# Performance work log

Hardware: AMD Instinct MI355X
Metric: run time of the kernel (lower is better)

Reference implementation:

```python
import math
import jax, jax.numpy as jnp
import numpy as np

CAPACITY_FACTOR = 1.0
MIN_CAPACITY = 8


def setup_inputs() -> dict:
    key = jax.random.key(0)
    k1, k2 = jax.random.split(key)
    s, d, e = 8192, 1024, 64
    inputs = jax.random.normal(k1, (s, d), dtype=jnp.float32)
    wg_weight = jax.random.normal(k2, (e, d), dtype=jnp.float32) * (1.0 / math.sqrt(d))
    return {"inputs": inputs, "wg_weight": wg_weight}


def reference(inputs, wg_weight):
    # gate projection (always fp32 in the original)
    logits = inputs.astype(jnp.float32) @ wg_weight.T  # [s, e]
    s, e = logits.shape
    # static capacity: ceil(s/e * capacity_factor), floored at min_capacity
    capacity = max(int(math.ceil(s / e * CAPACITY_FACTOR)), MIN_CAPACITY)

    gates = jax.nn.softmax(logits, axis=1)            # [s, e]
    indices = jnp.argmax(gates, axis=1)               # [s]
    mask = jax.nn.one_hot(indices, e, dtype=jnp.int32)  # [s, e]
    exp_counts = jnp.sum(mask, axis=0)                # [e]

    # load-balancing aux loss (uses mask BEFORE capacity dropping)
    me = jnp.mean(gates, axis=0)
    ce = jnp.mean(mask.astype(jnp.float32), axis=0)
    l_aux = jnp.sum(me * ce) * e

    # capacity dropping: with use_rts=False, topk over the binary mask keeps
    # the first `capacity` tokens routed to each expert, i.e. cumulative
    # position-in-expert < capacity
    positions = jnp.cumsum(mask, axis=0) - 1          # [s, e]
    mask = mask * (positions < capacity).astype(jnp.int32)

    locations = jnp.cumsum(mask, axis=0) - 1          # [s, e]
    locations_s = jnp.sum(locations * mask, axis=1)   # [s] slot per token

    gates = gates * mask.astype(jnp.float32)          # zero out dropped tokens
    locations_sc = jax.nn.one_hot(locations_s, capacity, dtype=jnp.float32)  # [s, c]
    combine_weights = jnp.einsum('se,sc->sec', gates, locations_sc)  # [s, e, c]
    dispatch_mask = combine_weights.astype(bool)
    return l_aux, combine_weights, dispatch_mask, exp_counts
```

## Files before the change

kernel.cpp:

```cpp
#include <hip/hip_runtime.h>
#include <cstdint>
#include <cstddef>

#define S 8192
#define Dm 1024
#define E 64
#define CAP 128
#define SEC 67108864ull

#define GEMM_BLOCKS 256
#define FILL_BLOCKS 1792
#define B0 16777217u
#define TCH 16777231u
#define CH 9363u
#define N4END 33554448u
#define WSCALE 4096.0f
#define INV_WSCALE (1.0f / 4096.0f)

typedef float f32x4 __attribute__((ext_vector_type(4)));
typedef _Float16 f16x4 __attribute__((ext_vector_type(4)));
typedef _Float16 f16x8 __attribute__((ext_vector_type(8)));

#define CV4(H, L, ROW, COL, V, SCALE) do {                                     \
    f16x4 hh, ll; float t_;                                                    \
    t_ = (V).x * (SCALE); hh[0] = (_Float16)t_; ll[0] = (_Float16)(t_ - (float)hh[0]); \
    t_ = (V).y * (SCALE); hh[1] = (_Float16)t_; ll[1] = (_Float16)(t_ - (float)hh[1]); \
    t_ = (V).z * (SCALE); hh[2] = (_Float16)t_; ll[2] = (_Float16)(t_ - (float)hh[2]); \
    t_ = (V).w * (SCALE); hh[3] = (_Float16)t_; ll[3] = (_Float16)(t_ - (float)hh[3]); \
    *(f16x4*)&H[ROW][COL] = hh;                                                \
    *(f16x4*)&L[ROW][COL] = ll;                                                \
} while (0)

__global__ __launch_bounds__(512) void k_main(const float* __restrict__ x,
                                              const float* __restrict__ w,
                                              float* __restrict__ gate,
                                              int* __restrict__ idx,
                                              float* __restrict__ me_part,
                                              int* __restrict__ cnt_g,
                                              float* __restrict__ la_ws,
                                              float* __restrict__ out) {
    int bid = blockIdx.x;
    int tid = threadIdx.x;
    if (bid < GEMM_BLOCKS) {
        __shared__ _Float16 Ah[32][72];
        __shared__ _Float16 Alo[32][72];
        __shared__ _Float16 Wh[64][72];
        __shared__ _Float16 Wlo[64][72];
        __shared__ float Sl[32][66];
        __shared__ float sm[32];
        __shared__ float sinv[32];
        __shared__ int sidx[32];
        int t0 = bid * 32;
        int ar = tid >> 4;
        int ac = (tid & 15) * 4;
        int wr = tid >> 3;
        int wc = (tid & 7) * 8;
        const float* asrc = x + (size_t)(t0 + ar) * Dm + ac;
        const float* wsrc = w + (size_t)wr * Dm + wc;

        int wv = tid >> 6;
        int l = tid & 63;
        int lr = l & 15;
        int lg = l >> 4;
        int mt = wv & 1;
        int nt = wv >> 1;
        f32x4 acc = {0.f, 0.f, 0.f, 0.f};

        float4 pa = *(const float4*)(asrc + 0);
        float4 pw0 = *(const float4*)(wsrc + 0);
        float4 pw1 = *(const float4*)(wsrc + 4);
        float4 qa = *(const float4*)(asrc + 64);
        float4 qw0 = *(const float4*)(wsrc + 64);
        float4 qw1 = *(const float4*)(wsrc + 68);

#define WRITE_LDS(A, W0, W1)                                                   \
        CV4(Ah, Alo, ar, ac, A, 1.0f);                                         \
        CV4(Wh, Wlo, wr, wc, W0, WSCALE);                                      \
        CV4(Wh, Wlo, wr, (wc + 4), W1, WSCALE);
#define LOADP(KB)                                                              \
        pa = *(const float4*)(asrc + (KB));                                    \
        pw0 = *(const float4*)(wsrc + (KB));                                   \
        pw1 = *(const float4*)(wsrc + (KB) + 4);
#define LOADQ(KB)                                                              \
        qa = *(const float4*)(asrc + (KB));                                    \
        qw0 = *(const float4*)(wsrc + (KB));                                   \
        qw1 = *(const float4*)(wsrc + (KB) + 4);
#define INNER_MFMA                                                             \
        _Pragma("unroll")                                                      \
        for (int ks = 0; ks < 2; ++ks) {                                       \
            int kc = ks * 32 + lg * 8;                                         \
            f16x8 ah = *(const f16x8*)&Ah[mt * 16 + lr][kc];                   \
            f16x8 al = *(const f16x8*)&Alo[mt * 16 + lr][kc];                  \
            f16x8 bh = *(const f16x8*)&Wh[nt * 16 + lr][kc];                   \
            f16x8 bl = *(const f16x8*)&Wlo[nt * 16 + lr][kc];                  \
            acc = __builtin_amdgcn_mfma_f32_16x16x32_f16(ah, bh, acc, 0, 0, 0); \
            acc = __builtin_amdgcn_mfma_f32_16x16x32_f16(al, bh, acc, 0, 0, 0); \
            acc = __builtin_amdgcn_mfma_f32_16x16x32_f16(ah, bl, acc, 0, 0, 0); \
        }

        for (int ch = 0; ch < 16; ch += 2) {
            __syncthreads();
            WRITE_LDS(pa, pw0, pw1)
            __syncthreads();
            if (ch + 2 < 16) { LOADP((ch + 2) * 64) }
            INNER_MFMA
            __syncthreads();
            WRITE_LDS(qa, qw0, qw1)
            __syncthreads();
            if (ch + 3 < 16) { LOADQ((ch + 3) * 64) }
            INNER_MFMA
        }
#undef WRITE_LDS
#undef LOADP
#undef LOADQ
#undef INNER_MFMA
        __syncthreads();
#pragma unroll
        for (int r = 0; r < 4; ++r)
            Sl[mt * 16 + lg * 4 + r][nt * 16 + lr] = acc[r] * INV_WSCALE;
        __syncthreads();
        if (tid < 32) {
            float m = Sl[tid][0];
            int am = 0;
#pragma unroll
            for (int c = 1; c < E; ++c) {
                float v = Sl[tid][c];
                if (v > m) { m = v; am = c; }
            }
            float ssum = 0.f;
#pragma unroll
            for (int c = 0; c < E; ++c) ssum += __expf(Sl[tid][c] - m);
            float inv = 1.0f / ssum;
            gate[t0 + tid] = inv;
            idx[t0 + tid] = am;
            sm[tid] = m;
            sinv[tid] = inv;
            sidx[tid] = am;
        }
        __syncthreads();
        if (tid < E) {
            float cs = 0.f;
            int cnt = 0;
#pragma unroll 8
            for (int r = 0; r < 32; ++r) {
                cs += __expf(Sl[r][tid] - sm[r]) * sinv[r];
                cnt += (sidx[r] == tid) ? 1 : 0;
            }
            me_part[bid * E + tid] = cs;
            cnt_g[bid * E + tid] = cnt;
        }
    } else {
        int fb = bid - GEMM_BLOCKS;
        if (fb == 0 && tid == 0) {
            out[1 + SEC] = 0.f; out[2 + SEC] = 0.f; out[3 + SEC] = 0.f;
            la_ws[0] = 0.f;
        }
        unsigned base = B0 + (unsigned)fb * CH;
        f32x4 z = {0.f, 0.f, 0.f, 0.f};
        f32x4* o4 = (f32x4*)out;
        for (unsigned j = tid; j < CH; j += 512u) {
            unsigned i = base + j;
            if (i < N4END) o4[i] = z;
        }
    }
}

__global__ __launch_bounds__(256) void k_scan(const int* __restrict__ idx,
                                              const float* __restrict__ gate,
                                              const float* __restrict__ me_part,
                                              const int* __restrict__ cnt_g,
                                              float2* __restrict__ tg,
                                              float* __restrict__ la_ws,
                                              float* __restrict__ out) {
    int e = blockIdx.x >> 2;
    int q = blockIdx.x & 3;
    int tid = threadIdx.x;
    int lane = tid & 63;
    int wid = tid >> 6;
    __shared__ int wsum[4];
    __shared__ int ired[256];
    __shared__ float red[256];
    int nb = q << 6;
    int a = 0;
    for (int b = tid; b < nb; b += 256) a += cnt_g[b * E + e];
    ired[tid] = a;
    __syncthreads();
    for (int s2 = 128; s2 > 0; s2 >>= 1) {
        if (tid < s2) ired[tid] += ired[tid + s2];
        __syncthreads();
    }
    int running = ired[0];
    __syncthreads();
    for (int ch = 0; ch < 8; ++ch) {
        int t = q * 2048 + ch * 256 + tid;
        bool f = (idx[t] == e);
        unsigned long long b = __ballot(f);
        int pre = __popcll(b & ((1ull << lane) - 1ull));
        if (lane == 0) wsum[wid] = __popcll(b);
        __syncthreads();
        int off = running;
#pragma unroll
        for (int w2 = 0; w2 < 4; ++w2)
            if (w2 < wid) off += wsum[w2];
        int p = off + pre;
        if (f) {
            int tgt = (p < CAP) ? e * CAP + p : -1;
            tg[t] = make_float2(__int_as_float(tgt), gate[t]);
        }
        running += wsum[0] + wsum[1] + wsum[2] + wsum[3];
        __syncthreads();
    }
    if (q == 3) {
        red[tid] = me_part[tid * E + e];
        __syncthreads();
        for (int s2 = 128; s2 > 0; s2 >>= 1) {
            if (tid < s2) red[tid] += red[tid + s2];
            __syncthreads();
        }
        if (tid == 0) {
            out[1 + 2 * (size_t)SEC + e] = (float)running;
            float la = red[0] * (1.0f / (float)S) *
                       ((float)running / (float)S) * (float)E;
            atomicAdd(la_ws, la);
        }
    }
}

__global__ __launch_bounds__(256) void k_merge(const float2* __restrict__ tg,
                                               const float* __restrict__ la_ws,
                                               float* __restrict__ out) {
    int bid = blockIdx.x;
    int tid = threadIdx.x;
    if (bid == 0 && tid == 0) out[0] = la_ws[0];
    f32x4* o4 = (f32x4*)out;
#pragma unroll
    for (int k = 0; k < 4; ++k) {
        int t = bid * 4 + k;
        float2 g = tg[t];
        int tgt = __float_as_int(g.x);
        float gv = g.y;
        for (int j = 1 + tid; j < 2048; j += 256) {
            int base = 4 * j - 1;
            f32x4 v;
            v[0] = (tgt == base) ? gv : 0.f;
            v[1] = (tgt == base + 1) ? gv : 0.f;
            v[2] = (tgt == base + 2) ? gv : 0.f;
            v[3] = (tgt == base + 3) ? gv : 0.f;
            o4[2048u * (unsigned)t + (unsigned)j] = v;
        }
        if (tid < 4) {
            int c = (tid < 3) ? tid : 8191;
            out[1 + (size_t)t * 8192 + c] = (tgt == c) ? gv : 0.f;
        }
        if (tid == 4 && tgt >= 0)
            out[1 + SEC + (size_t)t * 8192 + tgt] = 1.0f;
    }
}

extern "C" void kernel_launch(void* const* d_in, const int* in_sizes, int n_in,
                              void* d_out, int out_size, void* d_ws, size_t ws_size,
                              hipStream_t stream) {
    const float* x = (const float*)d_in[0];
    const float* w = (const float*)d_in[1];
    float* out = (float*)d_out;

    float* me_part = (float*)d_ws;
    float* gate = me_part + GEMM_BLOCKS * E;
    int* idx = (int*)(gate + S);
    int* cnt_g = idx + S;
    float2* tg = (float2*)(cnt_g + GEMM_BLOCKS * E);
    float* la_ws = (float*)(tg + S);

    k_main<<<dim3(GEMM_BLOCKS + FILL_BLOCKS), dim3(512), 0, stream>>>(
        x, w, gate, idx, me_part, cnt_g, la_ws, out);
    k_scan<<<dim3(256), dim3(256), 0, stream>>>(
        idx, gate, me_part, cnt_g, tg, la_ws, out);
    k_merge<<<dim3(2048), dim3(256), 0, stream>>>(tg, la_ws, out);
}
```

Before: 128.9 us.

## Halve GEMM tile to 16 tokens with 256-thread blocks and rebalance fill blocks

The fused gate-GEMM/zero-fill kernel now uses 256-thread blocks, each handling 16 tokens instead of 32. That doubles the number of GEMM blocks to 512 and reduces fill blocks to 1536 with a larger chunk each. Each wave computes one 16-column expert slice, and the weight tile is loaded as four row-strided float4s per thread. The scan kernel is adjusted for the larger number of per-block partial counts and sums. The aim is more parallelism for the GEMM part, at the cost of reloading the full weight tile twice as often per token.

```diff
diff --git a/kernel.cpp b/kernel.cpp
--- a/kernel.cpp
+++ b/kernel.cpp
@@ -8,11 +8,10 @@
 #define CAP 128
 #define SEC 67108864ull
 
-#define GEMM_BLOCKS 256
-#define FILL_BLOCKS 1792
+#define GEMM_BLOCKS 512
+#define FILL_BLOCKS 1536
 #define B0 16777217u
-#define TCH 16777231u
-#define CH 9363u
+#define CH 10923u
 #define N4END 33554448u
 #define WSCALE 4096.0f
 #define INV_WSCALE (1.0f / 4096.0f)
@@ -31,7 +30,7 @@
     *(f16x4*)&L[ROW][COL] = ll;                                                \
 } while (0)
 
-__global__ __launch_bounds__(512) void k_main(const float* __restrict__ x,
+__global__ __launch_bounds__(256) void k_main(const float* __restrict__ x,
                                               const float* __restrict__ w,
                                               float* __restrict__ gate,
                                               int* __restrict__ idx,
@@ -42,84 +41,83 @@
     int bid = blockIdx.x;
     int tid = threadIdx.x;
     if (bid < GEMM_BLOCKS) {
-        __shared__ _Float16 Ah[32][72];
-        __shared__ _Float16 Alo[32][72];
+        __shared__ _Float16 Ah[16][72];
+        __shared__ _Float16 Alo[16][72];
         __shared__ _Float16 Wh[64][72];
         __shared__ _Float16 Wlo[64][72];
-        __shared__ float Sl[32][66];
-        __shared__ float sm[32];
-        __shared__ float sinv[32];
-        __shared__ int sidx[32];
-        int t0 = bid * 32;
+        __shared__ float Sl[16][66];
+        __shared__ float sm[16];
+        __shared__ float sinv[16];
+        __shared__ int sidx[16];
+        int t0 = bid * 16;
         int ar = tid >> 4;
         int ac = (tid & 15) * 4;
-        int wr = tid >> 3;
-        int wc = (tid & 7) * 8;
         const float* asrc = x + (size_t)(t0 + ar) * Dm + ac;
-        const float* wsrc = w + (size_t)wr * Dm + wc;
+        const float* wsrc = w + (size_t)(tid >> 4) * Dm + (tid & 15) * 4;
 
         int wv = tid >> 6;
         int l = tid & 63;
         int lr = l & 15;
         int lg = l >> 4;
-        int mt = wv & 1;
-        int nt = wv >> 1;
         f32x4 acc = {0.f, 0.f, 0.f, 0.f};
 
-        float4 pa = *(const float4*)(asrc + 0);
-        float4 pw0 = *(const float4*)(wsrc + 0);
-        float4 pw1 = *(const float4*)(wsrc + 4);
-        float4 qa = *(const float4*)(asrc + 64);
-        float4 qw0 = *(const float4*)(wsrc + 64);
-        float4 qw1 = *(const float4*)(wsrc + 68);
-
-#define WRITE_LDS(A, W0, W1)                                                   \
-        CV4(Ah, Alo, ar, ac, A, 1.0f);                                         \
-        CV4(Wh, Wlo, wr, wc, W0, WSCALE);                                      \
-        CV4(Wh, Wlo, wr, (wc + 4), W1, WSCALE);
+        float4 pa, pw0, pw1, pw2, pw3;
+        float4 qa, qw0, qw1, qw2, qw3;
 #define LOADP(KB)                                                              \
         pa = *(const float4*)(asrc + (KB));                                    \
         pw0 = *(const float4*)(wsrc + (KB));                                   \
-        pw1 = *(const float4*)(wsrc + (KB) + 4);
+        pw1 = *(const float4*)(wsrc + 16 * (size_t)Dm + (KB));                 \
+        pw2 = *(const float4*)(wsrc + 32 * (size_t)Dm + (KB));                 \
+        pw3 = *(const float4*)(wsrc + 48 * (size_t)Dm + (KB));
 #define LOADQ(KB)                                                              \
         qa = *(const float4*)(asrc + (KB));                                    \
         qw0 = *(const float4*)(wsrc + (KB));                                   \
-        qw1 = *(const float4*)(wsrc + (KB) + 4);
+        qw1 = *(const float4*)(wsrc + 16 * (size_t)Dm + (KB));                 \
+        qw2 = *(const float4*)(wsrc + 32 * (size_t)Dm + (KB));                 \
+        qw3 = *(const float4*)(wsrc + 48 * (size_t)Dm + (KB));
+#define WRITE_LDS(A, W0, W1, W2, W3)                                           \
+        CV4(Ah, Alo, ar, ac, A, 1.0f);                                         \
+        CV4(Wh, Wlo, (tid >> 4), ((tid & 15) * 4), W0, WSCALE);                \
+        CV4(Wh, Wlo, (16 + (tid >> 4)), ((tid & 15) * 4), W1, WSCALE);         \
+        CV4(Wh, Wlo, (32 + (tid >> 4)), ((tid & 15) * 4), W2, WSCALE);         \
+        CV4(Wh, Wlo, (48 + (tid >> 4)), ((tid & 15) * 4), W3, WSCALE);
 #define INNER_MFMA                                                             \
         _Pragma("unroll")                                                      \
         for (int ks = 0; ks < 2; ++ks) {                                       \
             int kc = ks * 32 + lg * 8;                                         \
-            f16x8 ah = *(const f16x8*)&Ah[mt * 16 + lr][kc];                   \
-            f16x8 al = *(const f16x8*)&Alo[mt * 16 + lr][kc];                  \
-            f16x8 bh = *(const f16x8*)&Wh[nt * 16 + lr][kc];                   \
-            f16x8 bl = *(const f16x8*)&Wlo[nt * 16 + lr][kc];                  \
+            f16x8 ah = *(const f16x8*)&Ah[lr][kc];                             \
+            f16x8 al = *(const f16x8*)&Alo[lr][kc];                            \
+            f16x8 bh = *(const f16x8*)&Wh[wv * 16 + lr][kc];                   \
+            f16x8 bl = *(const f16x8*)&Wlo[wv * 16 + lr][kc];                  \
             acc = __builtin_amdgcn_mfma_f32_16x16x32_f16(ah, bh, acc, 0, 0, 0); \
             acc = __builtin_amdgcn_mfma_f32_16x16x32_f16(al, bh, acc, 0, 0, 0); \
             acc = __builtin_amdgcn_mfma_f32_16x16x32_f16(ah, bl, acc, 0, 0, 0); \
         }
 
+        LOADP(0)
+        LOADQ(64)
         for (int ch = 0; ch < 16; ch += 2) {
             __syncthreads();
-            WRITE_LDS(pa, pw0, pw1)
+            WRITE_LDS(pa, pw0, pw1, pw2, pw3)
             __syncthreads();
             if (ch + 2 < 16) { LOADP((ch + 2) * 64) }
             INNER_MFMA
             __syncthreads();
-            WRITE_LDS(qa, qw0, qw1)
+            WRITE_LDS(qa, qw0, qw1, qw2, qw3)
             __syncthreads();
             if (ch + 3 < 16) { LOADQ((ch + 3) * 64) }
             INNER_MFMA
         }
-#undef WRITE_LDS
 #undef LOADP
 #undef LOADQ
+#undef WRITE_LDS
 #undef INNER_MFMA
         __syncthreads();
 #pragma unroll
         for (int r = 0; r < 4; ++r)
-            Sl[mt * 16 + lg * 4 + r][nt * 16 + lr] = acc[r] * INV_WSCALE;
-        __syncthreads();
-        if (tid < 32) {
+            Sl[lg * 4 + r][wv * 16 + lr] = acc[r] * INV_WSCALE;
+        __syncthreads();
+        if (tid < 16) {
             float m = Sl[tid][0];
             int am = 0;
 #pragma unroll
@@ -141,8 +139,8 @@
         if (tid < E) {
             float cs = 0.f;
             int cnt = 0;
-#pragma unroll 8
-            for (int r = 0; r < 32; ++r) {
+#pragma unroll
+            for (int r = 0; r < 16; ++r) {
                 cs += __expf(Sl[r][tid] - sm[r]) * sinv[r];
                 cnt += (sidx[r] == tid) ? 1 : 0;
             }
@@ -158,7 +156,7 @@
         unsigned base = B0 + (unsigned)fb * CH;
         f32x4 z = {0.f, 0.f, 0.f, 0.f};
         f32x4* o4 = (f32x4*)out;
-        for (unsigned j = tid; j < CH; j += 512u) {
+        for (unsigned j = tid; j < CH; j += 256u) {
             unsigned i = base + j;
             if (i < N4END) o4[i] = z;
         }
@@ -180,7 +178,7 @@
     __shared__ int wsum[4];
     __shared__ int ired[256];
     __shared__ float red[256];
-    int nb = q << 6;
+    int nb = q << 7;
     int a = 0;
     for (int b = tid; b < nb; b += 256) a += cnt_g[b * E + e];
     ired[tid] = a;
@@ -211,7 +209,7 @@
         __syncthreads();
     }
     if (q == 3) {
-        red[tid] = me_part[tid * E + e];
+        red[tid] = me_part[tid * E + e] + me_part[(tid + 256) * E + e];
         __syncthreads();
         for (int s2 = 128; s2 > 0; s2 >>= 1) {
             if (tid < s2) red[tid] += red[tid + s2];
@@ -271,7 +269,7 @@
     float2* tg = (float2*)(cnt_g + GEMM_BLOCKS * E);
     float* la_ws = (float*)(tg + S);
 
-    k_main<<<dim3(GEMM_BLOCKS + FILL_BLOCKS), dim3(512), 0, stream>>>(
+    k_main<<<dim3(GEMM_BLOCKS + FILL_BLOCKS), dim3(256), 0, stream>>>(
         x, w, gate, idx, me_part, cnt_g, la_ws, out);
     k_scan<<<dim3(256), dim3(256), 0, stream>>>(
         idx, gate, me_part, cnt_g, tg, la_ws, out);
```

Measured after the change: 133.7 us. 3.7% more time.

## Stream fp32 tiles to LDS via global_load_lds double buffering with swizzle

Applied to the files above, without the earlier changes.

Replaces the register-staged global loads and fp16 hi/lo conversion-before-LDS with direct global-to-LDS asynchronous loads of raw fp32 tiles into a double-buffered, XOR-swizzled layout. The hi/lo fp16 split is now done per wave after reading from LDS, just before the MFMAs. This is meant to overlap the next chunk's memory traffic with compute and cut VGPR staging and barrier overhead. The cost is more LDS traffic (fp32 instead of fp16) and redundant conversion work, since each wave converts the tiles it reads.

```diff
diff --git a/kernel.cpp b/kernel.cpp
--- a/kernel.cpp
+++ b/kernel.cpp
@@ -11,24 +11,33 @@
 #define GEMM_BLOCKS 256
 #define FILL_BLOCKS 1792
 #define B0 16777217u
-#define TCH 16777231u
 #define CH 9363u
 #define N4END 33554448u
 #define WSCALE 4096.0f
 #define INV_WSCALE (1.0f / 4096.0f)
 
 typedef float f32x4 __attribute__((ext_vector_type(4)));
-typedef _Float16 f16x4 __attribute__((ext_vector_type(4)));
 typedef _Float16 f16x8 __attribute__((ext_vector_type(8)));
 
-#define CV4(H, L, ROW, COL, V, SCALE) do {                                     \
-    f16x4 hh, ll; float t_;                                                    \
-    t_ = (V).x * (SCALE); hh[0] = (_Float16)t_; ll[0] = (_Float16)(t_ - (float)hh[0]); \
-    t_ = (V).y * (SCALE); hh[1] = (_Float16)t_; ll[1] = (_Float16)(t_ - (float)hh[1]); \
-    t_ = (V).z * (SCALE); hh[2] = (_Float16)t_; ll[2] = (_Float16)(t_ - (float)hh[2]); \
-    t_ = (V).w * (SCALE); hh[3] = (_Float16)t_; ll[3] = (_Float16)(t_ - (float)hh[3]); \
-    *(f16x4*)&H[ROW][COL] = hh;                                                \
-    *(f16x4*)&L[ROW][COL] = ll;                                                \
+#define GLOAD(G, L) __builtin_amdgcn_global_load_lds(                          \
+    (const __attribute__((address_space(1))) void*)(G),                        \
+    (__attribute__((address_space(3))) void*)(L), 16, 0, 0)
+
+#define RAWBAR                                                                 \
+    asm volatile("s_waitcnt lgkmcnt(0)" ::: "memory");                         \
+    __builtin_amdgcn_sched_barrier(0);                                         \
+    __builtin_amdgcn_s_barrier();                                              \
+    __builtin_amdgcn_sched_barrier(0);
+
+#define CVT8(H, L, V0, V1, SC) do { float t_;                                  \
+    t_ = (V0).x * (SC); H[0] = (_Float16)t_; L[0] = (_Float16)(t_ - (float)H[0]); \
+    t_ = (V0).y * (SC); H[1] = (_Float16)t_; L[1] = (_Float16)(t_ - (float)H[1]); \
+    t_ = (V0).z * (SC); H[2] = (_Float16)t_; L[2] = (_Float16)(t_ - (float)H[2]); \
+    t_ = (V0).w * (SC); H[3] = (_Float16)t_; L[3] = (_Float16)(t_ - (float)H[3]); \
+    t_ = (V1).x * (SC); H[4] = (_Float16)t_; L[4] = (_Float16)(t_ - (float)H[4]); \
+    t_ = (V1).y * (SC); H[5] = (_Float16)t_; L[5] = (_Float16)(t_ - (float)H[5]); \
+    t_ = (V1).z * (SC); H[6] = (_Float16)t_; L[6] = (_Float16)(t_ - (float)H[6]); \
+    t_ = (V1).w * (SC); H[7] = (_Float16)t_; L[7] = (_Float16)(t_ - (float)H[7]); \
 } while (0)
 
 __global__ __launch_bounds__(512) void k_main(const float* __restrict__ x,
@@ -42,78 +51,75 @@
     int bid = blockIdx.x;
     int tid = threadIdx.x;
     if (bid < GEMM_BLOCKS) {
-        __shared__ _Float16 Ah[32][72];
-        __shared__ _Float16 Alo[32][72];
-        __shared__ _Float16 Wh[64][72];
-        __shared__ _Float16 Wlo[64][72];
+        __shared__ float Af[2][32 * 64];
+        __shared__ float Wf[2][64 * 64];
         __shared__ float Sl[32][66];
         __shared__ float sm[32];
         __shared__ float sinv[32];
         __shared__ int sidx[32];
         int t0 = bid * 32;
-        int ar = tid >> 4;
-        int ac = (tid & 15) * 4;
-        int wr = tid >> 3;
-        int wc = (tid & 7) * 8;
-        const float* asrc = x + (size_t)(t0 + ar) * Dm + ac;
-        const float* wsrc = w + (size_t)wr * Dm + wc;
-
         int wv = tid >> 6;
         int l = tid & 63;
+
+        int sar = tid >> 4;
+        int sacl = (tid & 15) ^ ((sar & 7) << 1);
+        const float* aga = x + (size_t)(t0 + sar) * Dm + sacl * 4;
+        int w1r = tid >> 4;
+        int w1cl = (tid & 15) ^ ((w1r & 7) << 1);
+        int w2r = 32 + (tid >> 4);
+        int w2cl = (tid & 15) ^ ((w2r & 7) << 1);
+        const float* wg1 = w + (size_t)w1r * Dm + w1cl * 4;
+        const float* wg2 = w + (size_t)w2r * Dm + w2cl * 4;
+
         int lr = l & 15;
         int lg = l >> 4;
         int mt = wv & 1;
         int nt = wv >> 1;
+        int ra = mt * 16 + lr;
+        int rw = nt * 16 + lr;
+        int mrow = (lr & 7) << 1;
         f32x4 acc = {0.f, 0.f, 0.f, 0.f};
 
-        float4 pa = *(const float4*)(asrc + 0);
-        float4 pw0 = *(const float4*)(wsrc + 0);
-        float4 pw1 = *(const float4*)(wsrc + 4);
-        float4 qa = *(const float4*)(asrc + 64);
-        float4 qw0 = *(const float4*)(wsrc + 64);
-        float4 qw1 = *(const float4*)(wsrc + 68);
-
-#define WRITE_LDS(A, W0, W1)                                                   \
-        CV4(Ah, Alo, ar, ac, A, 1.0f);                                         \
-        CV4(Wh, Wlo, wr, wc, W0, WSCALE);                                      \
-        CV4(Wh, Wlo, wr, (wc + 4), W1, WSCALE);
-#define LOADP(KB)                                                              \
-        pa = *(const float4*)(asrc + (KB));                                    \
-        pw0 = *(const float4*)(wsrc + (KB));                                   \
-        pw1 = *(const float4*)(wsrc + (KB) + 4);
-#define LOADQ(KB)                                                              \
-        qa = *(const float4*)(asrc + (KB));                                    \
-        qw0 = *(const float4*)(wsrc + (KB));                                   \
-        qw1 = *(const float4*)(wsrc + (KB) + 4);
-#define INNER_MFMA                                                             \
-        _Pragma("unroll")                                                      \
-        for (int ks = 0; ks < 2; ++ks) {                                       \
-            int kc = ks * 32 + lg * 8;                                         \
-            f16x8 ah = *(const f16x8*)&Ah[mt * 16 + lr][kc];                   \
-            f16x8 al = *(const f16x8*)&Alo[mt * 16 + lr][kc];                  \
-            f16x8 bh = *(const f16x8*)&Wh[nt * 16 + lr][kc];                   \
-            f16x8 bl = *(const f16x8*)&Wlo[nt * 16 + lr][kc];                  \
-            acc = __builtin_amdgcn_mfma_f32_16x16x32_f16(ah, bh, acc, 0, 0, 0); \
-            acc = __builtin_amdgcn_mfma_f32_16x16x32_f16(al, bh, acc, 0, 0, 0); \
-            acc = __builtin_amdgcn_mfma_f32_16x16x32_f16(ah, bl, acc, 0, 0, 0); \
-        }
-
-        for (int ch = 0; ch < 16; ch += 2) {
-            __syncthreads();
-            WRITE_LDS(pa, pw0, pw1)
-            __syncthreads();
-            if (ch + 2 < 16) { LOADP((ch + 2) * 64) }
-            INNER_MFMA
-            __syncthreads();
-            WRITE_LDS(qa, qw0, qw1)
-            __syncthreads();
-            if (ch + 3 < 16) { LOADQ((ch + 3) * 64) }
-            INNER_MFMA
-        }
-#undef WRITE_LDS
-#undef LOADP
-#undef LOADQ
-#undef INNER_MFMA
+#define ISSUE(B, KB)                                                           \
+        GLOAD(aga + (KB), &Af[B][wv * 256]);                                   \
+        GLOAD(wg1 + (KB), &Wf[B][wv * 256]);                                   \
+        GLOAD(wg2 + (KB), &Wf[B][2048 + wv * 256]);
+
+        ISSUE(0, 0)
+        ISSUE(1, 64)
+        asm volatile("s_waitcnt vmcnt(3)" ::: "memory");
+        __builtin_amdgcn_sched_barrier(0);
+        __builtin_amdgcn_s_barrier();
+        __builtin_amdgcn_sched_barrier(0);
+
+        for (int ch = 0; ch < 16; ++ch) {
+            int B = ch & 1;
+#pragma unroll
+            for (int ks = 0; ks < 2; ++ks) {
+                int cp = (ks * 8 + lg * 2) ^ mrow;
+                const float4* Ap = (const float4*)&Af[B][(size_t)ra * 64 + cp * 4];
+                float4 a0 = Ap[0], a1 = Ap[1];
+                const float4* Wp = (const float4*)&Wf[B][(size_t)rw * 64 + cp * 4];
+                float4 b0 = Wp[0], b1 = Wp[1];
+                f16x8 ah, al2, bh, bl;
+                CVT8(ah, al2, a0, a1, 1.0f);
+                CVT8(bh, bl, b0, b1, WSCALE);
+                acc = __builtin_amdgcn_mfma_f32_16x16x32_f16(ah, bh, acc, 0, 0, 0);
+                acc = __builtin_amdgcn_mfma_f32_16x16x32_f16(al2, bh, acc, 0, 0, 0);
+                acc = __builtin_amdgcn_mfma_f32_16x16x32_f16(ah, bl, acc, 0, 0, 0);
+            }
+            RAWBAR
+            if (ch + 2 < 16) { ISSUE(B, (ch + 2) * 64) }
+            if (ch + 1 < 16) {
+                if (ch + 2 < 16) {
+                    asm volatile("s_waitcnt vmcnt(3)" ::: "memory");
+                } else {
+                    asm volatile("s_waitcnt vmcnt(0)" ::: "memory");
+                }
+            }
+            RAWBAR
+        }
+#undef ISSUE
         __syncthreads();
 #pragma unroll
         for (int r = 0; r < 4; ++r)
```

Measured after the change: 130.9 us. No clear change (+1.5%).

## Fuse capacity scan into merge kernel, computing per-token slots locally

Applied to the files above, without the earlier changes.

Removes the separate k_scan kernel and its tg/la_ws workspace round trip. Each merge block now computes each token's position-in-expert itself: it sums per-GEMM-block expert counts for earlier blocks and uses a ballot over earlier tokens in the same 32-token block. One extra block reduces the counts and gate means to write exp_counts and l_aux directly, which drops the atomic. This saves a kernel launch and a serial dependency at the cost of redundant count reads in every merge block.

```diff
diff --git a/kernel.cpp b/kernel.cpp
--- a/kernel.cpp
+++ b/kernel.cpp
@@ -11,7 +11,6 @@
 #define GEMM_BLOCKS 256
 #define FILL_BLOCKS 1792
 #define B0 16777217u
-#define TCH 16777231u
 #define CH 9363u
 #define N4END 33554448u
 #define WSCALE 4096.0f
@@ -37,7 +36,6 @@
                                               int* __restrict__ idx,
                                               float* __restrict__ me_part,
                                               int* __restrict__ cnt_g,
-                                              float* __restrict__ la_ws,
                                               float* __restrict__ out) {
     int bid = blockIdx.x;
     int tid = threadIdx.x;
@@ -153,7 +151,6 @@
         int fb = bid - GEMM_BLOCKS;
         if (fb == 0 && tid == 0) {
             out[1 + SEC] = 0.f; out[2 + SEC] = 0.f; out[3 + SEC] = 0.f;
-            la_ws[0] = 0.f;
         }
         unsigned base = B0 + (unsigned)fb * CH;
         f32x4 z = {0.f, 0.f, 0.f, 0.f};
@@ -165,80 +162,69 @@
     }
 }
 
-__global__ __launch_bounds__(256) void k_scan(const int* __restrict__ idx,
-                                              const float* __restrict__ gate,
-                                              const float* __restrict__ me_part,
-                                              const int* __restrict__ cnt_g,
-                                              float2* __restrict__ tg,
-                                              float* __restrict__ la_ws,
-                                              float* __restrict__ out) {
-    int e = blockIdx.x >> 2;
-    int q = blockIdx.x & 3;
-    int tid = threadIdx.x;
-    int lane = tid & 63;
-    int wid = tid >> 6;
-    __shared__ int wsum[4];
-    __shared__ int ired[256];
-    __shared__ float red[256];
-    int nb = q << 6;
-    int a = 0;
-    for (int b = tid; b < nb; b += 256) a += cnt_g[b * E + e];
-    ired[tid] = a;
-    __syncthreads();
-    for (int s2 = 128; s2 > 0; s2 >>= 1) {
-        if (tid < s2) ired[tid] += ired[tid + s2];
-        __syncthreads();
-    }
-    int running = ired[0];
-    __syncthreads();
-    for (int ch = 0; ch < 8; ++ch) {
-        int t = q * 2048 + ch * 256 + tid;
-        bool f = (idx[t] == e);
-        unsigned long long b = __ballot(f);
-        int pre = __popcll(b & ((1ull << lane) - 1ull));
-        if (lane == 0) wsum[wid] = __popcll(b);
-        __syncthreads();
-        int off = running;
-#pragma unroll
-        for (int w2 = 0; w2 < 4; ++w2)
-            if (w2 < wid) off += wsum[w2];
-        int p = off + pre;
-        if (f) {
-            int tgt = (p < CAP) ? e * CAP + p : -1;
-            tg[t] = make_float2(__int_as_float(tgt), gate[t]);
-        }
-        running += wsum[0] + wsum[1] + wsum[2] + wsum[3];
-        __syncthreads();
-    }
-    if (q == 3) {
-        red[tid] = me_part[tid * E + e];
-        __syncthreads();
-        for (int s2 = 128; s2 > 0; s2 >>= 1) {
-            if (tid < s2) red[tid] += red[tid + s2];
-            __syncthreads();
-        }
-        if (tid == 0) {
-            out[1 + 2 * (size_t)SEC + e] = (float)running;
-            float la = red[0] * (1.0f / (float)S) *
-                       ((float)running / (float)S) * (float)E;
-            atomicAdd(la_ws, la);
-        }
-    }
-}
-
-__global__ __launch_bounds__(256) void k_merge(const float2* __restrict__ tg,
-                                               const float* __restrict__ la_ws,
+__global__ __launch_bounds__(256) void k_merge(const int* __restrict__ idx,
+                                               const float* __restrict__ gate,
+                                               const float* __restrict__ me_part,
+                                               const int* __restrict__ cnt_g,
                                                float* __restrict__ out) {
     int bid = blockIdx.x;
     int tid = threadIdx.x;
-    if (bid == 0 && tid == 0) out[0] = la_ws[0];
+    if (bid == 2048) {
+        __shared__ int ic[4][64];
+        __shared__ float fc[4][64];
+        int e = tid & 63, q = tid >> 6;
+        int cnt = 0; float me = 0.f;
+        for (int b = q * 64; b < q * 64 + 64; ++b) {
+            cnt += cnt_g[b * E + e];
+            me += me_part[b * E + e];
+        }
+        ic[q][e] = cnt; fc[q][e] = me;
+        __syncthreads();
+        if (tid < E) {
+            int c2 = ic[0][tid] + ic[1][tid] + ic[2][tid] + ic[3][tid];
+            float m2 = fc[0][tid] + fc[1][tid] + fc[2][tid] + fc[3][tid];
+            out[1 + 2 * (size_t)SEC + tid] = (float)c2;
+            float la = m2 * (1.0f / (float)S) * ((float)c2 / (float)S) * (float)E;
+#pragma unroll
+            for (int off = 32; off > 0; off >>= 1)
+                la += __shfl_down(la, off, 64);
+            if (tid == 0) out[0] = la;
+        }
+        return;
+    }
+    __shared__ int stg[4];
+    __shared__ float sgv[4];
+    {
+        int k = tid >> 6;
+        int lane = tid & 63;
+        int t = bid * 4 + k;
+        int e = idx[t];
+        int B = t >> 5;
+        int r = t & 31;
+        int pre = 0;
+#pragma unroll
+        for (int c = 0; c < 4; ++c) {
+            int b = lane + c * 64;
+            if (b < B) pre += cnt_g[b * E + e];
+        }
+#pragma unroll
+        for (int off = 32; off > 0; off >>= 1)
+            pre += __shfl_down(pre, off, 64);
+        bool m = (lane < r) && (idx[(B << 5) + lane] == e);
+        int rank = __popcll(__ballot(m));
+        if (lane == 0) {
+            int p = pre + rank;
+            stg[k] = (p < CAP) ? e * CAP + p : -1;
+            sgv[k] = gate[t];
+        }
+    }
+    __syncthreads();
     f32x4* o4 = (f32x4*)out;
 #pragma unroll
     for (int k = 0; k < 4; ++k) {
         int t = bid * 4 + k;
-        float2 g = tg[t];
-        int tgt = __float_as_int(g.x);
-        float gv = g.y;
+        int tgt = stg[k];
+        float gv = sgv[k];
         for (int j = 1 + tid; j < 2048; j += 256) {
             int base = 4 * j - 1;
             f32x4 v;
@@ -268,12 +254,9 @@
     float* gate = me_part + GEMM_BLOCKS * E;
     int* idx = (int*)(gate + S);
     int* cnt_g = idx + S;
-    float2* tg = (float2*)(cnt_g + GEMM_BLOCKS * E);
-    float* la_ws = (float*)(tg + S);
 
     k_main<<<dim3(GEMM_BLOCKS + FILL_BLOCKS), dim3(512), 0, stream>>>(
-        x, w, gate, idx, me_part, cnt_g, la_ws, out);
-    k_scan<<<dim3(256), dim3(256), 0, stream>>>(
-        idx, gate, me_part, cnt_g, tg, la_ws, out);
-    k_merge<<<dim3(2048), dim3(256), 0, stream>>>(tg, la_ws, out);
+        x, w, gate, idx, me_part, cnt_g, out);
+    k_merge<<<dim3(2049), dim3(256), 0, stream>>>(
+        idx, gate, me_part, cnt_g, out);
 }
```

After: 144.9 us. 12.3% more time.
